# Kernel optimization log

Hardware: AMD Instinct MI355X
Metric: run time of the kernel (lower is better)

The kernel has to match this reference:

```python
import jax, jax.numpy as jnp
import numpy as np

N = 50000      # nodes
E = 800000     # edges (avg degree 16)
IN = 256       # in_feats
H = 128        # hidden_feats
C = 40         # out_feats == num classes (label dim)
LPA_ITERS = 10


def setup_inputs() -> dict:
    key = jax.random.key(0)
    ks = jax.random.split(key, 9)
    features = jax.random.normal(ks[0], (N, IN), dtype=jnp.float32)
    labels = jax.random.normal(ks[1], (N, C), dtype=jnp.float32)
    mask = jax.random.randint(ks[2], (N,), 0, 2) > 0          # bool [N]
    src = jax.random.randint(ks[3], (E,), 0, N, dtype=jnp.int32)
    dst = jax.random.randint(ks[4], (E,), 0, N, dtype=jnp.int32)
    W1 = jax.random.normal(ks[5], (IN, H), dtype=jnp.float32) * (1.0 / np.sqrt(IN))
    b1 = jnp.zeros((H,), dtype=jnp.float32)
    W2 = jax.random.normal(ks[6], (H, C), dtype=jnp.float32) * (1.0 / np.sqrt(H))
    b2 = jnp.zeros((C,), dtype=jnp.float32)
    return {"features": features, "labels": labels, "mask": mask,
            "src": src, "dst": dst, "W1": W1, "b1": b1, "W2": W2, "b2": b2}


def reference(features, labels, mask, src, dst, W1, b1, W2, b2):
    ones_e = jnp.ones((E,), dtype=jnp.float32)
    deg_out = jax.ops.segment_sum(ones_e, src, num_segments=N)  # out-degree
    deg_in = jax.ops.segment_sum(ones_e, dst, num_segments=N)   # in-degree
    norm_src = jnp.maximum(deg_out, 1.0) ** -0.5                 # DGL clamps deg>=1
    norm_dst = jnp.maximum(deg_in, 1.0) ** -0.5

    def gconv(x, W, b):
        # DGL GraphConv, norm='both': D_in^{-1/2} A^T D_out^{-1/2} (x W) + b
        h = (x @ W) * norm_src[:, None]                          # [N, d_out]
        agg = jax.ops.segment_sum(h[src], dst, num_segments=N)   # gather+scatter-add
        return agg * norm_dst[:, None] + b

    x = jax.nn.relu(gconv(features, W1, b1))
    # dropout identity in eval mode
    x = gconv(x, W2, b2)

    # Label propagation: adj[src,dst]=1 so (adj @ y)[i] = sum_{(i->j)} y[j]
    masked_labels = jnp.where(mask[:, None], labels, 0.0)

    def step(y, _):
        y = jax.ops.segment_sum(y[dst], src, num_segments=N)
        y = jnp.where(mask[:, None], labels, y)
        return y, None

    y, _ = jax.lax.scan(step, masked_labels, None, length=LPA_ITERS)
    return x, y
```

## Files before the change

### kernel.cpp

```cpp
#include <hip/hip_runtime.h>

#define Nn 50000
#define Ee 800000
#define INF_ 256
#define HID 128
#define NC 40
#define CAPD 48
#define CAPS 48
#define LPA_ITERS 10
#define NB 98
#define BSH 9
#define EPB 1024
#define NBLK ((Ee + EPB - 1) / EPB)
#define G1_ROWS 64
#define G1BLK ((Nn + G1_ROWS - 1) / G1_ROWS)
#define CAPB_D 10240
#define CAPB_S 6144
#define AGG1_BLKS 2500
#define LPA_BLKS ((Nn + 31) / 32)
#define GEMM2_BLKS ((Nn + 319) / 320)

typedef __attribute__((ext_vector_type(8))) short bfrag;
typedef __attribute__((ext_vector_type(4))) float ffrag;

__device__ inline unsigned f2bf2(float a, float b) {
    unsigned ua = __float_as_uint(a); ua += 0x7FFFu + ((ua >> 16) & 1u);
    unsigned ub = __float_as_uint(b); ub += 0x7FFFu + ((ub >> 16) & 1u);
    return (ua >> 16) | (ub & 0xFFFF0000u);
}
__device__ inline unsigned short f2bf(float a) {
    unsigned ua = __float_as_uint(a); ua += 0x7FFFu + ((ua >> 16) & 1u);
    return (unsigned short)(ua >> 16);
}
__device__ inline float bf_lo(unsigned u) { return __uint_as_float(u << 16); }
__device__ inline float bf_hi(unsigned u) { return __uint_as_float(u & 0xFFFF0000u); }

__device__ inline bool read_mask(const void* mask, int node, int fmt) {
    if (fmt) return ((const unsigned char*)mask)[node] != 0;
    return ((const int*)mask)[node] != 0;
}

__global__ __launch_bounds__(256) void detect_prep(
    const unsigned int* __restrict__ m, int* flag,
    const float* __restrict__ W1, unsigned short* __restrict__ W1t) {
    int bb = blockIdx.x, tid = threadIdx.x;
    if (bb < 49) {
        int i = bb * 256 + tid;
        if (i < 12500) {
            if (m[i] > 1u) atomicOr(flag, 1);
        }
    } else {
        int c = bb - 49;
        W1t[c * INF_ + tid] = f2bf(W1[(size_t)tid * HID + c]);
    }
}

__global__ __launch_bounds__(256) void phase1(
    const int* __restrict__ src, const int* __restrict__ dst,
    const void* __restrict__ mask, const int* __restrict__ flag,
    int* __restrict__ cnt_src, int* __restrict__ cur_d, int* __restrict__ cur_s,
    unsigned* __restrict__ bkt_d, unsigned* __restrict__ bkt_s,
    const float* __restrict__ feat, const unsigned short* __restrict__ W1t,
    unsigned short* __restrict__ h1b) {
    __shared__ uint4 smem[784];
    const int tid = threadIdx.x;
    if (blockIdx.x < NBLK) {
        unsigned* stage_d = (unsigned*)smem;
        unsigned* stage_s = stage_d + EPB;
        int* hd  = (int*)(stage_s + EPB);
        int* od  = hd + NB;
        int* cd  = od + NB + 1;
        int* gd_ = cd + NB;
        int* hs  = gd_ + NB;
// ... 91 lines not shown
        for (int t = 0; t < 8; t++) acc[t] = (ffrag){0.f, 0.f, 0.f, 0.f};

        for (int k0 = 0; k0 < INF_; k0 += 32) {
#pragma unroll
            for (int p = 0; p < 2; p++) {
                int idx = tid + p * 256;
                int r = idx >> 3, c4 = idx & 7;
                int grow = row0 + r;
                float4 v = make_float4(0.f, 0.f, 0.f, 0.f);
                if (grow < Nn)
                    v = *(const float4*)(feat + (size_t)grow * INF_ + k0 + c4 * 4);
                uint2 pk;
                pk.x = f2bf2(v.x, v.y);
                pk.y = f2bf2(v.z, v.w);
                *(uint2*)((char*)lA + r * 64 + c4 * 8) = pk;
            }
#pragma unroll
            for (int p = 0; p < 2; p++) {
                int idx = tid + p * 256;
                int col = idx >> 2, q = idx & 3;
                uint4 v = *(const uint4*)((const char*)W1t + col * 512 + k0 * 2 + q * 16);
                *(uint4*)((char*)lB + col * 64 + q * 16) = v;
            }
            __syncthreads();
            int arow = rw0 + lane15;
            bfrag af = *(const bfrag*)((const char*)lA + arow * 64 + quad * 16);
#pragma unroll
            for (int t = 0; t < 8; t++) {
                int col = t * 16 + lane15;
                bfrag bf = *(const bfrag*)((const char*)lB + col * 64 + quad * 16);
                acc[t] = __builtin_amdgcn_mfma_f32_16x16x32_bf16(af, bf, acc[t], 0, 0, 0);
            }
            __syncthreads();
        }
#pragma unroll
        for (int t = 0; t < 8; t++) {
#pragma unroll
            for (int i = 0; i < 4; i++) {
                int grow = row0 + rw0 + quad * 4 + i;
                if (grow < Nn)
                    h1b[(size_t)grow * HID + t * 16 + lane15] = f2bf(acc[t][i]);
            }
        }
    }
}

__global__ __launch_bounds__(256) void build_csr_both(
    const unsigned* __restrict__ bkt_d, const int* __restrict__ cur_d,
    const unsigned* __restrict__ bkt_s, const int* __restrict__ cur_s,
    const void* __restrict__ mask, const int* __restrict__ flag,
    const int* __restrict__ cnt_src,
    int* __restrict__ adj_dst, int* __restrict__ cnt_dst,
    int* __restrict__ adj_s, int* __restrict__ cnt_u, int* __restrict__ cnt_m,
    float* __restrict__ nrm_s, int* __restrict__ n_un, int* __restrict__ ulist) {
    __shared__ int lu[512], lm[512];
    int bb = blockIdx.x, tid = threadIdx.x;
    lu[tid] = 0; lu[tid + 256] = 0; lm[tid] = 0; lm[tid + 256] = 0;
    __syncthreads();
    if (bb < NB) {
        int b = bb;
        int n = cur_d[b]; if (n > CAPB_D) n = CAPB_D;
        int n0 = b << BSH;
        const unsigned* base = bkt_d + (size_t)b * CAPB_D;
        for (int i = tid; i < n; i += 256) {
            unsigned r = base[i];
            int d = r >> 16, s = r & 0xffff;
            int sl = atomicAdd(&lu[d - n0], 1);
            if (sl < CAPD) adj_dst[d * CAPD + sl] = s;
        }
        __syncthreads();
        int g0 = n0 + tid;
        if (g0 < Nn) cnt_dst[g0] = lu[tid];
        g0 += 256;
        if (g0 < Nn) cnt_dst[g0] = lu[tid + 256];
    } else {
        int b = bb - NB;
        int fmt = *flag;
        int n = cur_s[b]; if (n > CAPB_S) n = CAPB_S;
        int n0 = b << BSH;
        const unsigned* base = bkt_s + (size_t)b * CAPB_S;
        for (int i = tid; i < n; i += 256) {
            unsigned r = base[i];
            int s = r >> 16, d = r & 0xffff;
            if (read_mask(mask, d, fmt)) {
                int sl = atomicAdd(&lm[s - n0], 1);
                if (sl < CAPS) adj_s[s * CAPS + (CAPS - 1 - sl)] = d;
            } else {
                int sl = atomicAdd(&lu[s - n0], 1);
                if (sl < CAPS) adj_s[s * CAPS + sl] = d;
            }
        }
        __syncthreads();
        int g0 = n0 + tid;
        if (g0 < Nn) {
            cnt_u[g0] = lu[tid]; cnt_m[g0] = lm[tid];
            int cs = cnt_src[g0];
            nrm_s[g0] = rsqrtf((float)(cs > 1 ? cs : 1));
            if (!read_mask(mask, g0, fmt)) {
                int p = atomicAdd(n_un, 1);
                ulist[p] = g0;
            }
        }
        g0 += 256;
        if (g0 < Nn) {
            cnt_u[g0] = lu[tid + 256]; cnt_m[g0] = lm[tid + 256];
            int cs = cnt_src[g0];
            nrm_s[g0] = rsqrtf((float)(cs > 1 ? cs : 1));
            if (!read_mask(mask, g0, fmt)) {
                int p = atomicAdd(n_un, 1);
                ulist[p] = g0;
            }
        }
    }
}


__device__ inline void do_agg1(
    int node, int l, const uint4* __restrict__ h1b,
    const int* __restrict__ adj_dst, const int* __restrict__ cnt_dst,
    const float* __restrict__ nrm_s, const float4* __restrict__ b1,
    float4* __restrict__ x1) {
    int dg = cnt_dst[node];
    int cnt = dg < CAPD ? dg : CAPD;
    const int* lst = adj_dst + (size_t)node * CAPD;
    float s0 = 0.f, s1 = 0.f, s2 = 0.f, s3 = 0.f;
    float s4 = 0.f, s5 = 0.f, s6 = 0.f, s7 = 0.f;
    int e = 0;
    for (; e + 8 <= cnt; e += 8) {
        uint4 u[8]; float ns[8];
#pragma unroll
        for (int q = 0; q < 8; q++) {
            int sidx = lst[e + q];
            u[q] = h1b[(size_t)sidx * 16 + l];
            ns[q] = nrm_s[sidx];
        }
#pragma unroll
        for (int q = 0; q < 8; q++) {
            s0 += ns[q] * bf_lo(u[q].x); s1 += ns[q] * bf_hi(u[q].x);
            s2 += ns[q] * bf_lo(u[q].y); s3 += ns[q] * bf_hi(u[q].y);
            s4 += ns[q] * bf_lo(u[q].z); s5 += ns[q] * bf_hi(u[q].z);
            s6 += ns[q] * bf_lo(u[q].w); s7 += ns[q] * bf_hi(u[q].w);
        }
    }
    for (; e < cnt; e++) {
        int sidx = lst[e];
        uint4 u = h1b[(size_t)sidx * 16 + l];
        float nsv = nrm_s[sidx];
        s0 += nsv * bf_lo(u.x); s1 += nsv * bf_hi(u.x);
        s2 += nsv * bf_lo(u.y); s3 += nsv * bf_hi(u.y);
        s4 += nsv * bf_lo(u.z); s5 += nsv * bf_hi(u.z);
        s6 += nsv * bf_lo(u.w); s7 += nsv * bf_hi(u.w);
    }
    float nrm = rsqrtf((float)(dg > 1 ? dg : 1));
    float4 bb0 = b1[l * 2], bb1 = b1[l * 2 + 1];
    float4 v0, v1;
    v0.x = fmaxf(s0 * nrm + bb0.x, 0.f);
    v0.y = fmaxf(s1 * nrm + bb0.y, 0.f);
    v0.z = fmaxf(s2 * nrm + bb0.z, 0.f);
    v0.w = fmaxf(s3 * nrm + bb0.w, 0.f);
    v1.x = fmaxf(s4 * nrm + bb1.x, 0.f);
    v1.y = fmaxf(s5 * nrm + bb1.y, 0.f);
    v1.z = fmaxf(s6 * nrm + bb1.z, 0.f);
    v1.w = fmaxf(s7 * nrm + bb1.w, 0.f);
    x1[(size_t)node * 32 + l * 2] = v0;
    x1[(size_t)node * 32 + l * 2 + 1] = v1;
}

__device__ inline void do_lpa_const(
    int g, int l, const float4* __restrict__ labels,
    const int* __restrict__ ulist, const int* __restrict__ adj_s,
    const int* __restrict__ cnt_m, float4* __restrict__ sconst,
    uint2* __restrict__ y1b) {
    int u = ulist[g];
    int cm = cnt_m[u];
    int cnt = cm < CAPS ? cm : CAPS;
    const int* lst = adj_s + (size_t)u * CAPS + (CAPS - cnt);
    float4 s = make_float4(0.f, 0.f, 0.f, 0.f);
    int e = 0;
    for (; e + 8 <= cnt; e += 8) {
        float4 v[8];
#pragma unroll
        for (int q = 0; q < 8; q++) v[q] = labels[(size_t)lst[e + q] * 10 + l];
#pragma unroll
        for (int q = 0; q < 8; q++) {
            s.x += v[q].x; s.y += v[q].y; s.z += v[q].z; s.w += v[q].w;
        }
    }
    for (; e + 4 <= cnt; e += 4) {
        float4 v[4];
#pragma unroll
        for (int q = 0; q < 4; q++) v[q] = labels[(size_t)lst[e + q] * 10 + l];
#pragma unroll
        for (int q = 0; q < 4; q++) {
            s.x += v[q].x; s.y += v[q].y; s.z += v[q].z; s.w += v[q].w;
        }
    }
    for (; e < cnt; e++) {
        float4 a = labels[(size_t)lst[e] * 10 + l];
        s.x += a.x; s.y += a.y; s.z += a.z; s.w += a.w;
    }
    sconst[(size_t)u * 10 + l] = s;
    uint2 pk; pk.x = f2bf2(s.x, s.y); pk.y = f2bf2(s.z, s.w);
    y1b[(size_t)u * 10 + l] = pk;
}

__device__ inline void do_lpa_mid(
    int g, int l, const uint2* __restrict__ ycur,
    const int* __restrict__ ulist, const int* __restrict__ adj_s,
    const int* __restrict__ cnt_u, const float4* __restrict__ sconst,
    uint2* __restrict__ ynext) {
    int u = ulist[g];
    int cu = cnt_u[u];
    int cnt = cu < CAPS ? cu : CAPS;
    const int* lst = adj_s + (size_t)u * CAPS;
    float4 s = sconst[(size_t)u * 10 + l];
    int e = 0;
    for (; e + 8 <= cnt; e += 8) {
        uint2 v[8];
#pragma unroll
// ... 17 lines not shown
    for (; e < cnt; e++) {
        uint2 v = ycur[(size_t)lst[e] * 10 + l];
        s.x += bf_lo(v.x); s.y += bf_hi(v.x);
        s.z += bf_lo(v.y); s.w += bf_hi(v.y);
    }
    uint2 pk; pk.x = f2bf2(s.x, s.y); pk.y = f2bf2(s.z, s.w);
    ynext[(size_t)u * 10 + l] = pk;
}

__device__ inline void do_agg2(
    int node, int l, const uint2* __restrict__ h2b,
    const int* __restrict__ adj_dst, const int* __restrict__ cnt_dst,
    const float4* __restrict__ b2, float4* __restrict__ out_x) {
    int dg = cnt_dst[node];
    int cnt = dg < CAPD ? dg : CAPD;
    const int* lst = adj_dst + (size_t)node * CAPD;
    float s0 = 0.f, s1 = 0.f, s2 = 0.f, s3 = 0.f;
    int e = 0;
    for (; e + 8 <= cnt; e += 8) {
        uint2 u[8];
#pragma unroll
        for (int q = 0; q < 8; q++) u[q] = h2b[(size_t)lst[e + q] * 10 + l];
#pragma unroll
        for (int q = 0; q < 8; q++) {
            s0 += bf_lo(u[q].x); s1 += bf_hi(u[q].x);
            s2 += bf_lo(u[q].y); s3 += bf_hi(u[q].y);
        }
    }
    for (; e + 4 <= cnt; e += 4) {
        uint2 u[4];
#pragma unroll
        for (int q = 0; q < 4; q++) u[q] = h2b[(size_t)lst[e + q] * 10 + l];
#pragma unroll
        for (int q = 0; q < 4; q++) {
            s0 += bf_lo(u[q].x); s1 += bf_hi(u[q].x);
            s2 += bf_lo(u[q].y); s3 += bf_hi(u[q].y);
        }
    }
    for (; e < cnt; e++) {
        uint2 u = h2b[(size_t)lst[e] * 10 + l];
        s0 += bf_lo(u.x); s1 += bf_hi(u.x);
        s2 += bf_lo(u.y); s3 += bf_hi(u.y);
    }
    float nrm = rsqrtf((float)(dg > 1 ? dg : 1));
    float4 bb = b2[l];
    float4 v;
    v.x = s0 * nrm + bb.x;
    v.y = s1 * nrm + bb.y;
    v.z = s2 * nrm + bb.z;
    v.w = s3 * nrm + bb.w;
    out_x[(size_t)node * 10 + l] = v;
}

__global__ __launch_bounds__(320) void k_agg1_lconst(
    const uint4* __restrict__ h1b, const int* __restrict__ adj_dst,
    const int* __restrict__ cnt_dst, const float* __restrict__ nrm_s,
    const float4* __restrict__ b1, float4* __restrict__ x1,
    const float4* __restrict__ labels, const void* __restrict__ mask,
    const int* __restrict__ flag, const int* __restrict__ n_un,
    const int* __restrict__ ulist, const int* __restrict__ adj_s,
    const int* __restrict__ cnt_m, float4* __restrict__ sconst,
    uint2* __restrict__ y1b, float4* __restrict__ out_y4) {
    int bb = blockIdx.x, tid = threadIdx.x;
    if (bb < AGG1_BLKS) {
        int node = bb * 20 + (tid >> 4);
        do_agg1(node, tid & 15, h1b, adj_dst, cnt_dst, nrm_s, b1, x1);
    } else {
        int lb = bb - AGG1_BLKS;
        int fmt = *flag;
        int i = lb * 320 + tid;
        if (i < Nn * 10) {
            int node = i / 10;
            if (read_mask(mask, node, fmt)) out_y4[i] = labels[i];
        }
        int g = lb * 32 + tid / 10;
        if (g < *n_un)
            do_lpa_const(g, tid % 10, labels, ulist, adj_s, cnt_m, sconst, y1b);
    }
}

__global__ __launch_bounds__(320) void k_gemm2_mid(
    const float4* __restrict__ x1, const float4* __restrict__ W2,
    const int* __restrict__ cnt_src, unsigned* __restrict__ h2b,
    const uint2* __restrict__ ycur, const int* __restrict__ n_un,
    const int* __restrict__ ulist, const int* __restrict__ adj_s,
    const int* __restrict__ cnt_u, const float4* __restrict__ sconst,
    uint2* __restrict__ ynext) {
    __shared__ float lw[HID * NC];
    int bb = blockIdx.x, tid = threadIdx.x;
    if (bb < GEMM2_BLKS) {
        for (int i = tid; i < HID * NC / 4; i += 320)
            ((float4*)lw)[i] = W2[i];
        __syncthreads();
        int r = bb * 320 + tid;
        if (r >= Nn) return;
        const float4* xr = x1 + (size_t)r * 32;
        float4 acc[10];
#pragma unroll
        for (int j = 0; j < 10; j++) acc[j] = make_float4(0.f, 0.f, 0.f, 0.f);
        for (int k4 = 0; k4 < 32; k4++) {
            float4 xv = xr[k4];
#pragma unroll
            for (int s = 0; s < 4; s++) {
                float x = s == 0 ? xv.x : (s == 1 ? xv.y : (s == 2 ? xv.z : xv.w));
                const float4* wrow = (const float4*)(lw + (k4 * 4 + s) * NC);
#pragma unroll
                for (int j = 0; j < 10; j++) {
                    float4 w = wrow[j];
                    acc[j].x += x * w.x; acc[j].y += x * w.y;
                    acc[j].z += x * w.z; acc[j].w += x * w.w;
                }
            }
        }
        int dg = cnt_src[r];
        float nrm = rsqrtf((float)(dg > 1 ? dg : 1));
        uint2* out = (uint2*)(h2b + (size_t)r * 20);
#pragma unroll
        for (int j = 0; j < 10; j++) {
            uint2 pk;
            pk.x = f2bf2(acc[j].x * nrm, acc[j].y * nrm);
            pk.y = f2bf2(acc[j].z * nrm, acc[j].w * nrm);
            out[j] = pk;
        }
    } else {
        int g = (bb - GEMM2_BLKS) * 32 + tid / 10;
        if (g < *n_un)
            do_lpa_mid(g, tid % 10, ycur, ulist, adj_s, cnt_u, sconst, ynext);
    }
}

__global__ __launch_bounds__(320) void k_agg2_mid(
    const uint2* __restrict__ h2b, const int* __restrict__ adj_dst,
    const int* __restrict__ cnt_dst, const float4* __restrict__ b2,
    float4* __restrict__ out_x,
    const uint2* __restrict__ ycur, const int* __restrict__ n_un,
    const int* __restrict__ ulist, const int* __restrict__ adj_s,
    const int* __restrict__ cnt_u, const float4* __restrict__ sconst,
    uint2* __restrict__ ynext) {
    int bb = blockIdx.x, tid = threadIdx.x;
    if (bb < LPA_BLKS) {
        int node = bb * 32 + tid / 10;
        if (node < Nn)
            do_agg2(node, tid % 10, h2b, adj_dst, cnt_dst, b2, out_x);
    } else {
        int g = (bb - LPA_BLKS) * 32 + tid / 10;
        if (g < *n_un)
            do_lpa_mid(g, tid % 10, ycur, ulist, adj_s, cnt_u, sconst, ynext);
    }
}

__global__ __launch_bounds__(320) void lpa_mid(
    const uint2* __restrict__ ycur, const int* __restrict__ n_un,
    const int* __restrict__ ulist, const int* __restrict__ adj_s,
    const int* __restrict__ cnt_u, const float4* __restrict__ sconst,
    uint2* __restrict__ ynext) {
    int g = blockIdx.x * 32 + threadIdx.x / 10;
    if (g < *n_un)
        do_lpa_mid(g, threadIdx.x % 10, ycur, ulist, adj_s, cnt_u, sconst, ynext);
}

__global__ __launch_bounds__(320) void lpa_last(
    const uint2* __restrict__ ycur, const int* __restrict__ n_un,
    const int* __restrict__ ulist, const int* __restrict__ adj_s,
    const int* __restrict__ cnt_u, const float4* __restrict__ sconst,
    float4* __restrict__ out_y) {
    int g = blockIdx.x * 32 + threadIdx.x / 10;
    int l = threadIdx.x % 10;
    if (g >= *n_un) return;
    int u = ulist[g];
    int cu = cnt_u[u];
    int cnt = cu < CAPS ? cu : CAPS;
    const int* lst = adj_s + (size_t)u * CAPS;
    float4 s = sconst[(size_t)u * 10 + l];
    int e = 0;
    for (; e + 8 <= cnt; e += 8) {
        uint2 v[8];
#pragma unroll
        for (int q = 0; q < 8; q++) v[q] = ycur[(size_t)lst[e + q] * 10 + l];
#pragma unroll
        for (int q = 0; q < 8; q++) {
            s.x += bf_lo(v[q].x); s.y += bf_hi(v[q].x);
            s.z += bf_lo(v[q].y); s.w += bf_hi(v[q].y);
        }
    }
    for (; e + 4 <= cnt; e += 4) {
        uint2 v[4];
#pragma unroll
        for (int q = 0; q < 4; q++) v[q] = ycur[(size_t)lst[e + q] * 10 + l];
#pragma unroll
        for (int q = 0; q < 4; q++) {
            s.x += bf_lo(v[q].x); s.y += bf_hi(v[q].x);
            s.z += bf_lo(v[q].y); s.w += bf_hi(v[q].y);
        }
    }
    for (; e < cnt; e++) {
        uint2 v = ycur[(size_t)lst[e] * 10 + l];
        s.x += bf_lo(v.x); s.y += bf_hi(v.x);
        s.z += bf_lo(v.y); s.w += bf_hi(v.y);
    }
    out_y[(size_t)u * 10 + l] = s;
}

extern "C" void kernel_launch(void* const* d_in, const int* in_sizes, int n_in,
                              void* d_out, int out_size, void* d_ws, size_t ws_size,
                              hipStream_t stream) {
    const float* feat   = (const float*)d_in[0];
    const float* labels = (const float*)d_in[1];
    const void*  mask   = d_in[2];
    const int*   src    = (const int*)d_in[3];
    const int*   dst    = (const int*)d_in[4];
    const float* W1     = (const float*)d_in[5];
    const float* b1     = (const float*)d_in[6];
    const float* W2     = (const float*)d_in[7];
    const float* b2     = (const float*)d_in[8];

    float* out_x = (float*)d_out;
    float* out_y = out_x + (size_t)Nn * NC;

    char* ws = (char*)d_ws;
    size_t off = 0;
    auto alloc = [&](size_t bytes) -> void* {
        void* p = ws + off;
        off += (bytes + 255) & ~(size_t)255;
        return p;
    };
    int* flag    = (int*)alloc(256);
    int* n_un    = flag + 1;
    int* cnt_src = (int*)alloc((size_t)Nn * 4);
    int* cur_d   = (int*)alloc(512);
    int* cur_s   = (int*)alloc(512);
    size_t zero_bytes = off;
    int* cnt_dst = (int*)alloc((size_t)Nn * 4);
    int* cnt_u   = (int*)alloc((size_t)Nn * 4);
    int* cnt_m   = (int*)alloc((size_t)Nn * 4);
    int* ulist   = (int*)alloc((size_t)Nn * 4);
    float* nrm_s = (float*)alloc((size_t)Nn * 4);
    unsigned short* W1t = (unsigned short*)alloc((size_t)HID * INF_ * 2);
    unsigned* bkt_d = (unsigned*)alloc((size_t)NB * CAPB_D * 4);
    unsigned* bkt_s = (unsigned*)alloc((size_t)NB * CAPB_S * 4);
    unsigned short* h1b = (unsigned short*)alloc((size_t)Nn * HID * 2);
    float* x1 = (float*)alloc((size_t)Nn * HID * 4);
    int* adj_s   = (int*)alloc((size_t)Nn * CAPS * 4);
    int* adj_dst = (int*)alloc((size_t)Nn * CAPD * 4);
    unsigned* h2b = (unsigned*)alloc((size_t)Nn * NC * 2);
    float* sconst = (float*)alloc((size_t)Nn * NC * 4);
    uint2* y1b = (uint2*)alloc((size_t)Nn * NC * 2);
    uint2* y2b = (uint2*)alloc((size_t)Nn * NC * 2);

    hipMemsetAsync(d_ws, 0, zero_bytes, stream);

    detect_prep<<<49 + HID, 256, 0, stream>>>((const unsigned int*)mask, flag,
                                              W1, W1t);
    phase1<<<NBLK + G1BLK, 256, 0, stream>>>(
        src, dst, mask, flag, cnt_src, cur_d, cur_s, bkt_d, bkt_s,
        feat, W1t, h1b);
    build_csr_both<<<NB * 2, 256, 0, stream>>>(
        bkt_d, cur_d, bkt_s, cur_s, mask, flag, cnt_src,
        adj_dst, cnt_dst, adj_s, cnt_u, cnt_m, nrm_s, n_un, ulist);

    k_agg1_lconst<<<AGG1_BLKS + LPA_BLKS, 320, 0, stream>>>(
        (const uint4*)h1b, adj_dst, cnt_dst, nrm_s, (const float4*)b1,
        (float4*)x1, (const float4*)labels, mask, flag, n_un, ulist, adj_s,
        cnt_m, (float4*)sconst, y1b, (float4*)out_y);
    k_gemm2_mid<<<GEMM2_BLKS + LPA_BLKS, 320, 0, stream>>>(
        (const float4*)x1, (const float4*)W2, cnt_src, h2b,
        y1b, n_un, ulist, adj_s, cnt_u, (const float4*)sconst, y2b);
    k_agg2_mid<<<LPA_BLKS + LPA_BLKS, 320, 0, stream>>>(
        (const uint2*)h2b, adj_dst, cnt_dst, (const float4*)b2, (float4*)out_x,
        y2b, n_un, ulist, adj_s, cnt_u, (const float4*)sconst, y1b);

    const uint2* cur = y1b;
    for (int i = 0; i < 6; i++) {
        uint2* nxt = (i & 1) ? y1b : y2b;
        lpa_mid<<<LPA_BLKS, 320, 0, stream>>>(
            cur, n_un, ulist, adj_s, cnt_u, (const float4*)sconst, nxt);
        cur = nxt;
    }
    lpa_last<<<LPA_BLKS, 320, 0, stream>>>(
        cur, n_un, ulist, adj_s, cnt_u, (const float4*)sconst, (float4*)out_y);
}
```

Baseline: 375.1 us.

## Fuse remaining LPA iterations into one cooperative kernel with grid sync

Replaces the six lpa_mid launches and the final lpa_last launch with one cooperative kernel. It runs a fixed grid of 768 blocks that loops over the unlabeled nodes and uses grid.sync() between iterations, ping-ponging the y buffers. This removes per-launch overhead and the drain and refill gaps between seven small kernels. In exchange it uses fewer resident blocks with grid-stride loops, and grid-wide barriers could reduce latency hiding for the gather-bound work.

```diff
diff --git a/kernel.cpp b/kernel.cpp
--- a/kernel.cpp
+++ b/kernel.cpp
@@ -1,4 +1,7 @@
 #include <hip/hip_runtime.h>
+#include <hip/hip_cooperative_groups.h>
+
+namespace cg = cooperative_groups;
 
 #define Nn 50000
 #define Ee 800000
@@ -19,6 +22,7 @@
 #define AGG1_BLKS 2500
 #define LPA_BLKS ((Nn + 31) / 32)
 #define GEMM2_BLKS ((Nn + 319) / 320)
+#define COOP_BLKS 768
 
 typedef __attribute__((ext_vector_type(8))) short bfrag;
 typedef __attribute__((ext_vector_type(4))) float ffrag;
@@ -549,56 +553,61 @@
     }
 }
 
-__global__ __launch_bounds__(320) void lpa_mid(
-    const uint2* __restrict__ ycur, const int* __restrict__ n_un,
-    const int* __restrict__ ulist, const int* __restrict__ adj_s,
-    const int* __restrict__ cnt_u, const float4* __restrict__ sconst,
-    uint2* __restrict__ ynext) {
-    int g = blockIdx.x * 32 + threadIdx.x / 10;
-    if (g < *n_un)
-        do_lpa_mid(g, threadIdx.x % 10, ycur, ulist, adj_s, cnt_u, sconst, ynext);
-}
-
-__global__ __launch_bounds__(320) void lpa_last(
-    const uint2* __restrict__ ycur, const int* __restrict__ n_un,
-    const int* __restrict__ ulist, const int* __restrict__ adj_s,
-    const int* __restrict__ cnt_u, const float4* __restrict__ sconst,
+__global__ __launch_bounds__(320) void lpa_coop(
+    const int* __restrict__ n_un, const int* __restrict__ ulist,
+    const int* __restrict__ adj_s, const int* __restrict__ cnt_u,
+    const float4* __restrict__ sconst,
+    uint2* __restrict__ ya, uint2* __restrict__ yb,
     float4* __restrict__ out_y) {
-    int g = blockIdx.x * 32 + threadIdx.x / 10;
-    int l = threadIdx.x % 10;
-    if (g >= *n_un) return;
-    int u = ulist[g];
-    int cu = cnt_u[u];
-    int cnt = cu < CAPS ? cu : CAPS;
-    const int* lst = adj_s + (size_t)u * CAPS;
-    float4 s = sconst[(size_t)u * 10 + l];
-    int e = 0;
-    for (; e + 8 <= cnt; e += 8) {
-        uint2 v[8];
-#pragma unroll
-        for (int q = 0; q < 8; q++) v[q] = ycur[(size_t)lst[e + q] * 10 + l];
-#pragma unroll
-        for (int q = 0; q < 8; q++) {
-            s.x += bf_lo(v[q].x); s.y += bf_hi(v[q].x);
-            s.z += bf_lo(v[q].y); s.w += bf_hi(v[q].y);
-        }
-    }
-    for (; e + 4 <= cnt; e += 4) {
-        uint2 v[4];
-#pragma unroll
-        for (int q = 0; q < 4; q++) v[q] = ycur[(size_t)lst[e + q] * 10 + l];
-#pragma unroll
-        for (int q = 0; q < 4; q++) {
-            s.x += bf_lo(v[q].x); s.y += bf_hi(v[q].x);
-            s.z += bf_lo(v[q].y); s.w += bf_hi(v[q].y);
-        }
-    }
-    for (; e < cnt; e++) {
-        uint2 v = ycur[(size_t)lst[e] * 10 + l];
-        s.x += bf_lo(v.x); s.y += bf_hi(v.x);
-        s.z += bf_lo(v.y); s.w += bf_hi(v.y);
-    }
-    out_y[(size_t)u * 10 + l] = s;
+    cg::grid_group grid = cg::this_grid();
+    const int nu = *n_un;
+    const int l = threadIdx.x % 10;
+    const int g0 = blockIdx.x * 32 + threadIdx.x / 10;
+    const int gstep = gridDim.x * 32;
+
+    const uint2* cur = ya;
+    uint2* nxt = yb;
+#pragma unroll 1
+    for (int it = 0; it < 6; it++) {
+        for (int g = g0; g < nu; g += gstep)
+            do_lpa_mid(g, l, cur, ulist, adj_s, cnt_u, sconst, nxt);
+        grid.sync();
+        const uint2* t = cur; cur = nxt; nxt = (uint2*)t;
+    }
+    for (int g = g0; g < nu; g += gstep) {
+        int u = ulist[g];
+        int cu = cnt_u[u];
+        int cnt = cu < CAPS ? cu : CAPS;
+        const int* lst = adj_s + (size_t)u * CAPS;
+        float4 s = sconst[(size_t)u * 10 + l];
+        int e = 0;
+        for (; e + 8 <= cnt; e += 8) {
+            uint2 v[8];
+#pragma unroll
+            for (int q = 0; q < 8; q++) v[q] = cur[(size_t)lst[e + q] * 10 + l];
+#pragma unroll
+            for (int q = 0; q < 8; q++) {
+                s.x += bf_lo(v[q].x); s.y += bf_hi(v[q].x);
+                s.z += bf_lo(v[q].y); s.w += bf_hi(v[q].y);
+            }
+        }
+        for (; e + 4 <= cnt; e += 4) {
+            uint2 v[4];
+#pragma unroll
+            for (int q = 0; q < 4; q++) v[q] = cur[(size_t)lst[e + q] * 10 + l];
+#pragma unroll
+            for (int q = 0; q < 4; q++) {
+                s.x += bf_lo(v[q].x); s.y += bf_hi(v[q].x);
+                s.z += bf_lo(v[q].y); s.w += bf_hi(v[q].y);
+            }
+        }
+        for (; e < cnt; e++) {
+            uint2 v = cur[(size_t)lst[e] * 10 + l];
+            s.x += bf_lo(v.x); s.y += bf_hi(v.x);
+            s.z += bf_lo(v.y); s.w += bf_hi(v.y);
+        }
+        out_y[(size_t)u * 10 + l] = s;
+    }
 }
 
 extern "C" void kernel_launch(void* const* d_in, const int* in_sizes, int n_in,
@@ -669,13 +678,17 @@
         (const uint2*)h2b, adj_dst, cnt_dst, (const float4*)b2, (float4*)out_x,
         y2b, n_un, ulist, adj_s, cnt_u, (const float4*)sconst, y1b);
 
-    const uint2* cur = y1b;
-    for (int i = 0; i < 6; i++) {
-        uint2* nxt = (i & 1) ? y1b : y2b;
-        lpa_mid<<<LPA_BLKS, 320, 0, stream>>>(
-            cur, n_un, ulist, adj_s, cnt_u, (const float4*)sconst, nxt);
-        cur = nxt;
-    }
-    lpa_last<<<LPA_BLKS, 320, 0, stream>>>(
-        cur, n_un, ulist, adj_s, cnt_u, (const float4*)sconst, (float4*)out_y);
-}
+    const int* n_un_c = n_un;
+    const int* ulist_c = ulist;
+    const int* adj_s_c = adj_s;
+    const int* cnt_u_c = cnt_u;
+    const float4* sconst_c = (const float4*)sconst;
+    uint2* ya = y1b;
+    uint2* yb = y2b;
+    float4* outy4 = (float4*)out_y;
+    void* cargs[] = {(void*)&n_un_c, (void*)&ulist_c, (void*)&adj_s_c,
+                     (void*)&cnt_u_c, (void*)&sconst_c, (void*)&ya,
+                     (void*)&yb, (void*)&outy4};
+    hipLaunchCooperativeKernel((void*)lpa_coop, dim3(COOP_BLKS), dim3(320),
+                               cargs, 0, stream);
+}
```

Measured after the change: 914.5 us. 2.44x slower.

## Fuse layer-1 aggregation with layer-2 GEMM and prescale h1 by source norm

Applied to the files above, without the earlier changes.

The layer-1 aggregation kernel now also computes the 128x40 W2 projection in shared memory per block of 20 nodes and writes bf16 h2 directly. This removes the fp32 x1 intermediate and the separate gemm2 kernel. The source-degree normalization is folded into h1 by extra blocks in the CSR build kernel, so the gather no longer loads nrm_s per edge. The LPA iteration that ran inside gemm2 is moved into the loop as an extra lpa_mid launch. The costs are an extra round of bf16 rounding on h1 and per-block W2 staging into shared memory, which raises LDS use and may lower occupancy.

```diff
diff --git a/kernel.cpp b/kernel.cpp
--- a/kernel.cpp
+++ b/kernel.cpp
@@ -18,7 +18,7 @@
 #define CAPB_S 6144
 #define AGG1_BLKS 2500
 #define LPA_BLKS ((Nn + 31) / 32)
-#define GEMM2_BLKS ((Nn + 319) / 320)
+#define SCB 196
 
 typedef __attribute__((ext_vector_type(8))) short bfrag;
 typedef __attribute__((ext_vector_type(4))) float ffrag;
@@ -216,7 +216,8 @@
     const int* __restrict__ cnt_src,
     int* __restrict__ adj_dst, int* __restrict__ cnt_dst,
     int* __restrict__ adj_s, int* __restrict__ cnt_u, int* __restrict__ cnt_m,
-    float* __restrict__ nrm_s, int* __restrict__ n_un, int* __restrict__ ulist) {
+    int* __restrict__ n_un, int* __restrict__ ulist,
+    unsigned short* __restrict__ h1b) {
     __shared__ int lu[512], lm[512];
     int bb = blockIdx.x, tid = threadIdx.x;
     lu[tid] = 0; lu[tid + 256] = 0; lm[tid] = 0; lm[tid + 256] = 0;
@@ -237,7 +238,7 @@
         if (g0 < Nn) cnt_dst[g0] = lu[tid];
         g0 += 256;
         if (g0 < Nn) cnt_dst[g0] = lu[tid + 256];
-    } else {
+    } else if (bb < 2 * NB) {
         int b = bb - NB;
         int fmt = *flag;
         int n = cur_s[b]; if (n > CAPB_S) n = CAPB_S;
@@ -258,8 +259,6 @@
         int g0 = n0 + tid;
         if (g0 < Nn) {
             cnt_u[g0] = lu[tid]; cnt_m[g0] = lm[tid];
-            int cs = cnt_src[g0];
-            nrm_s[g0] = rsqrtf((float)(cs > 1 ? cs : 1));
             if (!read_mask(mask, g0, fmt)) {
                 int p = atomicAdd(n_un, 1);
                 ulist[p] = g0;
@@ -268,67 +267,35 @@
         g0 += 256;
         if (g0 < Nn) {
             cnt_u[g0] = lu[tid + 256]; cnt_m[g0] = lm[tid + 256];
-            int cs = cnt_src[g0];
-            nrm_s[g0] = rsqrtf((float)(cs > 1 ? cs : 1));
             if (!read_mask(mask, g0, fmt)) {
                 int p = atomicAdd(n_un, 1);
                 ulist[p] = g0;
             }
         }
-    }
-}
-
-
-__device__ inline void do_agg1(
-    int node, int l, const uint4* __restrict__ h1b,
-    const int* __restrict__ adj_dst, const int* __restrict__ cnt_dst,
-    const float* __restrict__ nrm_s, const float4* __restrict__ b1,
-    float4* __restrict__ x1) {
-    int dg = cnt_dst[node];
-    int cnt = dg < CAPD ? dg : CAPD;
-    const int* lst = adj_dst + (size_t)node * CAPD;
-    float s0 = 0.f, s1 = 0.f, s2 = 0.f, s3 = 0.f;
-    float s4 = 0.f, s5 = 0.f, s6 = 0.f, s7 = 0.f;
-    int e = 0;
-    for (; e + 8 <= cnt; e += 8) {
-        uint4 u[8]; float ns[8];
-#pragma unroll
-        for (int q = 0; q < 8; q++) {
-            int sidx = lst[e + q];
-            u[q] = h1b[(size_t)sidx * 16 + l];
-            ns[q] = nrm_s[sidx];
-        }
-#pragma unroll
-        for (int q = 0; q < 8; q++) {
-            s0 += ns[q] * bf_lo(u[q].x); s1 += ns[q] * bf_hi(u[q].x);
-            s2 += ns[q] * bf_lo(u[q].y); s3 += ns[q] * bf_hi(u[q].y);
-            s4 += ns[q] * bf_lo(u[q].z); s5 += ns[q] * bf_hi(u[q].z);
-            s6 += ns[q] * bf_lo(u[q].w); s7 += ns[q] * bf_hi(u[q].w);
-        }
-    }
-    for (; e < cnt; e++) {
-        int sidx = lst[e];
-        uint4 u = h1b[(size_t)sidx * 16 + l];
-        float nsv = nrm_s[sidx];
-        s0 += nsv * bf_lo(u.x); s1 += nsv * bf_hi(u.x);
-        s2 += nsv * bf_lo(u.y); s3 += nsv * bf_hi(u.y);
-        s4 += nsv * bf_lo(u.z); s5 += nsv * bf_hi(u.z);
-        s6 += nsv * bf_lo(u.w); s7 += nsv * bf_hi(u.w);
-    }
-    float nrm = rsqrtf((float)(dg > 1 ? dg : 1));
-    float4 bb0 = b1[l * 2], bb1 = b1[l * 2 + 1];
-    float4 v0, v1;
-    v0.x = fmaxf(s0 * nrm + bb0.x, 0.f);
-    v0.y = fmaxf(s1 * nrm + bb0.y, 0.f);
-    v0.z = fmaxf(s2 * nrm + bb0.z, 0.f);
-    v0.w = fmaxf(s3 * nrm + bb0.w, 0.f);
-    v1.x = fmaxf(s4 * nrm + bb1.x, 0.f);
-    v1.y = fmaxf(s5 * nrm + bb1.y, 0.f);
-    v1.z = fmaxf(s6 * nrm + bb1.z, 0.f);
-    v1.w = fmaxf(s7 * nrm + bb1.w, 0.f);
-    x1[(size_t)node * 32 + l * 2] = v0;
-    x1[(size_t)node * 32 + l * 2 + 1] = v1;
-}
+    } else {
+        int b = bb - 2 * NB;
+        int rbase = b * 256;
+        int c8 = tid & 7;
+#pragma unroll 1
+        for (int it = 0; it < 8; it++) {
+            int r = rbase + it * 32 + (tid >> 3);
+            if (r >= Nn) continue;
+            int cs = cnt_src[r];
+            float nr = rsqrtf((float)(cs > 1 ? cs : 1));
+            uint4* row = (uint4*)(h1b + (size_t)r * HID);
+#pragma unroll
+            for (int h = 0; h < 2; h++) {
+                uint4 u = row[c8 * 2 + h];
+                u.x = f2bf2(bf_lo(u.x) * nr, bf_hi(u.x) * nr);
+                u.y = f2bf2(bf_lo(u.y) * nr, bf_hi(u.y) * nr);
+                u.z = f2bf2(bf_lo(u.z) * nr, bf_hi(u.z) * nr);
+                u.w = f2bf2(bf_lo(u.w) * nr, bf_hi(u.w) * nr);
+                row[c8 * 2 + h] = u;
+            }
+        }
+    }
+}
+
 
 __device__ inline void do_lpa_const(
     int g, int l, const float4* __restrict__ labels,
@@ -452,19 +419,96 @@
     out_x[(size_t)node * 10 + l] = v;
 }
 
-__global__ __launch_bounds__(320) void k_agg1_lconst(
+__global__ __launch_bounds__(320) void k_aggemm_lconst(
     const uint4* __restrict__ h1b, const int* __restrict__ adj_dst,
-    const int* __restrict__ cnt_dst, const float* __restrict__ nrm_s,
-    const float4* __restrict__ b1, float4* __restrict__ x1,
+    const int* __restrict__ cnt_dst, const int* __restrict__ cnt_src,
+    const float4* __restrict__ b1, const float* __restrict__ W2,
+    unsigned* __restrict__ h2b,
     const float4* __restrict__ labels, const void* __restrict__ mask,
     const int* __restrict__ flag, const int* __restrict__ n_un,
     const int* __restrict__ ulist, const int* __restrict__ adj_s,
     const int* __restrict__ cnt_m, float4* __restrict__ sconst,
     uint2* __restrict__ y1b, float4* __restrict__ out_y4) {
+    __shared__ float lsm[NC * 132 + 20 * 132];
     int bb = blockIdx.x, tid = threadIdx.x;
     if (bb < AGG1_BLKS) {
-        int node = bb * 20 + (tid >> 4);
-        do_agg1(node, tid & 15, h1b, adj_dst, cnt_dst, nrm_s, b1, x1);
+        float* lwt = lsm;
+        float* xs  = lsm + NC * 132;
+        for (int i = tid; i < HID * NC; i += 320) {
+            int k = i / NC, c = i % NC;
+            lwt[c * 132 + k] = W2[i];
+        }
+        __syncthreads();
+
+        const int slot = tid >> 4;
+        const int node = bb * 20 + slot;
+        const int l = tid & 15;
+        int dg = cnt_dst[node];
+        int cnt = dg < CAPD ? dg : CAPD;
+        const int* lst = adj_dst + (size_t)node * CAPD;
+        float s0 = 0.f, s1 = 0.f, s2 = 0.f, s3 = 0.f;
+        float s4 = 0.f, s5 = 0.f, s6 = 0.f, s7 = 0.f;
+        int e = 0;
+        for (; e + 8 <= cnt; e += 8) {
+            uint4 u[8];
+#pragma unroll
+            for (int q = 0; q < 8; q++) u[q] = h1b[(size_t)lst[e + q] * 16 + l];
+#pragma unroll
+            for (int q = 0; q < 8; q++) {
+                s0 += bf_lo(u[q].x); s1 += bf_hi(u[q].x);
+                s2 += bf_lo(u[q].y); s3 += bf_hi(u[q].y);
+                s4 += bf_lo(u[q].z); s5 += bf_hi(u[q].z);
+                s6 += bf_lo(u[q].w); s7 += bf_hi(u[q].w);
+            }
+        }
+        for (; e < cnt; e++) {
+            uint4 u = h1b[(size_t)lst[e] * 16 + l];
+            s0 += bf_lo(u.x); s1 += bf_hi(u.x);
+            s2 += bf_lo(u.y); s3 += bf_hi(u.y);
+            s4 += bf_lo(u.z); s5 += bf_hi(u.z);
+            s6 += bf_lo(u.w); s7 += bf_hi(u.w);
+        }
+        float nrm = rsqrtf((float)(dg > 1 ? dg : 1));
+        float4 bb0 = b1[l * 2], bb1 = b1[l * 2 + 1];
+        float4 v0, v1;
+        v0.x = fmaxf(s0 * nrm + bb0.x, 0.f);
+        v0.y = fmaxf(s1 * nrm + bb0.y, 0.f);
+        v0.z = fmaxf(s2 * nrm + bb0.z, 0.f);
+        v0.w = fmaxf(s3 * nrm + bb0.w, 0.f);
+        v1.x = fmaxf(s4 * nrm + bb1.x, 0.f);
+        v1.y = fmaxf(s5 * nrm + bb1.y, 0.f);
+        v1.z = fmaxf(s6 * nrm + bb1.z, 0.f);
+        v1.w = fmaxf(s7 * nrm + bb1.w, 0.f);
+        float* xrow = xs + slot * 132;
+        *(float4*)(xrow + l * 8) = v0;
+        *(float4*)(xrow + l * 8 + 4) = v1;
+        __syncthreads();
+
+        int c0 = l, c1 = l + 16;
+        const float* w0 = lwt + c0 * 132;
+        const float* w1 = lwt + c1 * 132;
+        const float* w2p = lwt + ((l < 8) ? (l + 32) : c0) * 132;
+        float a0 = 0.f, a1 = 0.f, a2 = 0.f;
+#pragma unroll 8
+        for (int k4 = 0; k4 < 32; k4++) {
+            float4 xv = *(const float4*)(xrow + k4 * 4);
+            float4 wa = *(const float4*)(w0 + k4 * 4);
+            float4 wb = *(const float4*)(w1 + k4 * 4);
+            float4 wc = *(const float4*)(w2p + k4 * 4);
+            a0 += xv.x * wa.x + xv.y * wa.y + xv.z * wa.z + xv.w * wa.w;
+            a1 += xv.x * wb.x + xv.y * wb.y + xv.z * wb.z + xv.w * wb.w;
+            a2 += xv.x * wc.x + xv.y * wc.y + xv.z * wc.z + xv.w * wc.w;
+        }
+        int dgs = cnt_src[node];
+        float nrm2 = rsqrtf((float)(dgs > 1 ? dgs : 1));
+        xrow[c0] = a0 * nrm2;
+        xrow[c1] = a1 * nrm2;
+        if (l < 8) xrow[l + 32] = a2 * nrm2;
+        if (l < 10) {
+            float4 p = *(const float4*)(xrow + l * 4);
+            uint2 pk; pk.x = f2bf2(p.x, p.y); pk.y = f2bf2(p.z, p.w);
+            ((uint2*)(h2b + (size_t)node * 20))[l] = pk;
+        }
     } else {
         int lb = bb - AGG1_BLKS;
         int fmt = *flag;
@@ -476,56 +520,6 @@
         int g = lb * 32 + tid / 10;
         if (g < *n_un)
             do_lpa_const(g, tid % 10, labels, ulist, adj_s, cnt_m, sconst, y1b);
-    }
-}
-
-__global__ __launch_bounds__(320) void k_gemm2_mid(
-    const float4* __restrict__ x1, const float4* __restrict__ W2,
-    const int* __restrict__ cnt_src, unsigned* __restrict__ h2b,
-    const uint2* __restrict__ ycur, const int* __restrict__ n_un,
-    const int* __restrict__ ulist, const int* __restrict__ adj_s,
-    const int* __restrict__ cnt_u, const float4* __restrict__ sconst,
-    uint2* __restrict__ ynext) {
-    __shared__ float lw[HID * NC];
-    int bb = blockIdx.x, tid = threadIdx.x;
-    if (bb < GEMM2_BLKS) {
-        for (int i = tid; i < HID * NC / 4; i += 320)
-            ((float4*)lw)[i] = W2[i];
-        __syncthreads();
-        int r = bb * 320 + tid;
-        if (r >= Nn) return;
-        const float4* xr = x1 + (size_t)r * 32;
-        float4 acc[10];
-#pragma unroll
-        for (int j = 0; j < 10; j++) acc[j] = make_float4(0.f, 0.f, 0.f, 0.f);
-        for (int k4 = 0; k4 < 32; k4++) {
-            float4 xv = xr[k4];
-#pragma unroll
-            for (int s = 0; s < 4; s++) {
-                float x = s == 0 ? xv.x : (s == 1 ? xv.y : (s == 2 ? xv.z : xv.w));
-                const float4* wrow = (const float4*)(lw + (k4 * 4 + s) * NC);
-#pragma unroll
-                for (int j = 0; j < 10; j++) {
-                    float4 w = wrow[j];
-                    acc[j].x += x * w.x; acc[j].y += x * w.y;
-                    acc[j].z += x * w.z; acc[j].w += x * w.w;
-                }
-            }
-        }
-        int dg = cnt_src[r];
-        float nrm = rsqrtf((float)(dg > 1 ? dg : 1));
-        uint2* out = (uint2*)(h2b + (size_t)r * 20);
-#pragma unroll
-        for (int j = 0; j < 10; j++) {
-            uint2 pk;
-            pk.x = f2bf2(acc[j].x * nrm, acc[j].y * nrm);
-            pk.y = f2bf2(acc[j].z * nrm, acc[j].w * nrm);
-            out[j] = pk;
-        }
-    } else {
-        int g = (bb - GEMM2_BLKS) * 32 + tid / 10;
-        if (g < *n_un)
-            do_lpa_mid(g, tid % 10, ycur, ulist, adj_s, cnt_u, sconst, ynext);
     }
 }
 
@@ -634,12 +628,10 @@
     int* cnt_u   = (int*)alloc((size_t)Nn * 4);
     int* cnt_m   = (int*)alloc((size_t)Nn * 4);
     int* ulist   = (int*)alloc((size_t)Nn * 4);
-    float* nrm_s = (float*)alloc((size_t)Nn * 4);
     unsigned short* W1t = (unsigned short*)alloc((size_t)HID * INF_ * 2);
     unsigned* bkt_d = (unsigned*)alloc((size_t)NB * CAPB_D * 4);
     unsigned* bkt_s = (unsigned*)alloc((size_t)NB * CAPB_S * 4);
     unsigned short* h1b = (unsigned short*)alloc((size_t)Nn * HID * 2);
-    float* x1 = (float*)alloc((size_t)Nn * HID * 4);
     int* adj_s   = (int*)alloc((size_t)Nn * CAPS * 4);
     int* adj_dst = (int*)alloc((size_t)Nn * CAPD * 4);
     unsigned* h2b = (unsigned*)alloc((size_t)Nn * NC * 2);
@@ -654,24 +646,21 @@
     phase1<<<NBLK + G1BLK, 256, 0, stream>>>(
         src, dst, mask, flag, cnt_src, cur_d, cur_s, bkt_d, bkt_s,
         feat, W1t, h1b);
-    build_csr_both<<<NB * 2, 256, 0, stream>>>(
+    build_csr_both<<<NB * 2 + SCB, 256, 0, stream>>>(
         bkt_d, cur_d, bkt_s, cur_s, mask, flag, cnt_src,
-        adj_dst, cnt_dst, adj_s, cnt_u, cnt_m, nrm_s, n_un, ulist);
-
-    k_agg1_lconst<<<AGG1_BLKS + LPA_BLKS, 320, 0, stream>>>(
-        (const uint4*)h1b, adj_dst, cnt_dst, nrm_s, (const float4*)b1,
-        (float4*)x1, (const float4*)labels, mask, flag, n_un, ulist, adj_s,
+        adj_dst, cnt_dst, adj_s, cnt_u, cnt_m, n_un, ulist, h1b);
+
+    k_aggemm_lconst<<<AGG1_BLKS + LPA_BLKS, 320, 0, stream>>>(
+        (const uint4*)h1b, adj_dst, cnt_dst, cnt_src, (const float4*)b1,
+        W2, h2b, (const float4*)labels, mask, flag, n_un, ulist, adj_s,
         cnt_m, (float4*)sconst, y1b, (float4*)out_y);
-    k_gemm2_mid<<<GEMM2_BLKS + LPA_BLKS, 320, 0, stream>>>(
-        (const float4*)x1, (const float4*)W2, cnt_src, h2b,
-        y1b, n_un, ulist, adj_s, cnt_u, (const float4*)sconst, y2b);
     k_agg2_mid<<<LPA_BLKS + LPA_BLKS, 320, 0, stream>>>(
         (const uint2*)h2b, adj_dst, cnt_dst, (const float4*)b2, (float4*)out_x,
-        y2b, n_un, ulist, adj_s, cnt_u, (const float4*)sconst, y1b);
-
-    const uint2* cur = y1b;
-    for (int i = 0; i < 6; i++) {
-        uint2* nxt = (i & 1) ? y1b : y2b;
+        y1b, n_un, ulist, adj_s, cnt_u, (const float4*)sconst, y2b);
+
+    const uint2* cur = y2b;
+    for (int i = 0; i < 7; i++) {
+        uint2* nxt = (i & 1) ? y2b : y1b;
         lpa_mid<<<LPA_BLKS, 320, 0, stream>>>(
             cur, n_un, ulist, adj_s, cnt_u, (const float4*)sconst, nxt);
         cur = nxt;
```

Result: faster. 367.7 us (-2.0%).

## Prescale h1 by source norm in place and store layer-1 activations as bf16

Applied to the files above, without the earlier changes.

Extra blocks in the CSR build kernel scale each bf16 h1 row in place by the source-degree norm. This removes the per-edge nrm_s gather from the layer-1 aggregation and drops the nrm_s array. The layer-1 output x1 is now written and read as bf16 instead of fp32, which halves its write and read traffic into the second GEMM. The cost is an extra read-modify-write pass over h1 and additional bf16 rounding, both on the prescaled h1 and on x1.

```diff
diff --git a/kernel.cpp b/kernel.cpp
--- a/kernel.cpp
+++ b/kernel.cpp
@@ -19,6 +19,7 @@
 #define AGG1_BLKS 2500
 #define LPA_BLKS ((Nn + 31) / 32)
 #define GEMM2_BLKS ((Nn + 319) / 320)
+#define SCB 196
 
 typedef __attribute__((ext_vector_type(8))) short bfrag;
 typedef __attribute__((ext_vector_type(4))) float ffrag;
@@ -216,7 +217,8 @@
     const int* __restrict__ cnt_src,
     int* __restrict__ adj_dst, int* __restrict__ cnt_dst,
     int* __restrict__ adj_s, int* __restrict__ cnt_u, int* __restrict__ cnt_m,
-    float* __restrict__ nrm_s, int* __restrict__ n_un, int* __restrict__ ulist) {
+    int* __restrict__ n_un, int* __restrict__ ulist,
+    unsigned short* __restrict__ h1b) {
     __shared__ int lu[512], lm[512];
     int bb = blockIdx.x, tid = threadIdx.x;
     lu[tid] = 0; lu[tid + 256] = 0; lm[tid] = 0; lm[tid + 256] = 0;
@@ -237,7 +239,7 @@
         if (g0 < Nn) cnt_dst[g0] = lu[tid];
         g0 += 256;
         if (g0 < Nn) cnt_dst[g0] = lu[tid + 256];
-    } else {
+    } else if (bb < 2 * NB) {
         int b = bb - NB;
         int fmt = *flag;
         int n = cur_s[b]; if (n > CAPB_S) n = CAPB_S;
@@ -258,8 +260,6 @@
         int g0 = n0 + tid;
         if (g0 < Nn) {
             cnt_u[g0] = lu[tid]; cnt_m[g0] = lm[tid];
-            int cs = cnt_src[g0];
-            nrm_s[g0] = rsqrtf((float)(cs > 1 ? cs : 1));
             if (!read_mask(mask, g0, fmt)) {
                 int p = atomicAdd(n_un, 1);
                 ulist[p] = g0;
@@ -268,67 +268,35 @@
         g0 += 256;
         if (g0 < Nn) {
             cnt_u[g0] = lu[tid + 256]; cnt_m[g0] = lm[tid + 256];
-            int cs = cnt_src[g0];
-            nrm_s[g0] = rsqrtf((float)(cs > 1 ? cs : 1));
             if (!read_mask(mask, g0, fmt)) {
                 int p = atomicAdd(n_un, 1);
                 ulist[p] = g0;
             }
         }
-    }
-}
-
-
-__device__ inline void do_agg1(
-    int node, int l, const uint4* __restrict__ h1b,
-    const int* __restrict__ adj_dst, const int* __restrict__ cnt_dst,
-    const float* __restrict__ nrm_s, const float4* __restrict__ b1,
-    float4* __restrict__ x1) {
-    int dg = cnt_dst[node];
-    int cnt = dg < CAPD ? dg : CAPD;
-    const int* lst = adj_dst + (size_t)node * CAPD;
-    float s0 = 0.f, s1 = 0.f, s2 = 0.f, s3 = 0.f;
-    float s4 = 0.f, s5 = 0.f, s6 = 0.f, s7 = 0.f;
-    int e = 0;
-    for (; e + 8 <= cnt; e += 8) {
-        uint4 u[8]; float ns[8];
-#pragma unroll
-        for (int q = 0; q < 8; q++) {
-            int sidx = lst[e + q];
-            u[q] = h1b[(size_t)sidx * 16 + l];
-            ns[q] = nrm_s[sidx];
-        }
-#pragma unroll
-        for (int q = 0; q < 8; q++) {
-            s0 += ns[q] * bf_lo(u[q].x); s1 += ns[q] * bf_hi(u[q].x);
-            s2 += ns[q] * bf_lo(u[q].y); s3 += ns[q] * bf_hi(u[q].y);
-            s4 += ns[q] * bf_lo(u[q].z); s5 += ns[q] * bf_hi(u[q].z);
-            s6 += ns[q] * bf_lo(u[q].w); s7 += ns[q] * bf_hi(u[q].w);
-        }
-    }
-    for (; e < cnt; e++) {
-        int sidx = lst[e];
-        uint4 u = h1b[(size_t)sidx * 16 + l];
-        float nsv = nrm_s[sidx];
-        s0 += nsv * bf_lo(u.x); s1 += nsv * bf_hi(u.x);
-        s2 += nsv * bf_lo(u.y); s3 += nsv * bf_hi(u.y);
-        s4 += nsv * bf_lo(u.z); s5 += nsv * bf_hi(u.z);
-        s6 += nsv * bf_lo(u.w); s7 += nsv * bf_hi(u.w);
-    }
-    float nrm = rsqrtf((float)(dg > 1 ? dg : 1));
-    float4 bb0 = b1[l * 2], bb1 = b1[l * 2 + 1];
-    float4 v0, v1;
-    v0.x = fmaxf(s0 * nrm + bb0.x, 0.f);
-    v0.y = fmaxf(s1 * nrm + bb0.y, 0.f);
-    v0.z = fmaxf(s2 * nrm + bb0.z, 0.f);
-    v0.w = fmaxf(s3 * nrm + bb0.w, 0.f);
-    v1.x = fmaxf(s4 * nrm + bb1.x, 0.f);
-    v1.y = fmaxf(s5 * nrm + bb1.y, 0.f);
-    v1.z = fmaxf(s6 * nrm + bb1.z, 0.f);
-    v1.w = fmaxf(s7 * nrm + bb1.w, 0.f);
-    x1[(size_t)node * 32 + l * 2] = v0;
-    x1[(size_t)node * 32 + l * 2 + 1] = v1;
-}
+    } else {
+        int b = bb - 2 * NB;
+        int rbase = b * 256;
+        int c8 = tid & 7;
+#pragma unroll 1
+        for (int it = 0; it < 8; it++) {
+            int r = rbase + it * 32 + (tid >> 3);
+            if (r >= Nn) continue;
+            int cs = cnt_src[r];
+            float nr = rsqrtf((float)(cs > 1 ? cs : 1));
+            uint4* row = (uint4*)(h1b + (size_t)r * HID);
+#pragma unroll
+            for (int h = 0; h < 2; h++) {
+                uint4 u = row[c8 * 2 + h];
+                u.x = f2bf2(bf_lo(u.x) * nr, bf_hi(u.x) * nr);
+                u.y = f2bf2(bf_lo(u.y) * nr, bf_hi(u.y) * nr);
+                u.z = f2bf2(bf_lo(u.z) * nr, bf_hi(u.z) * nr);
+                u.w = f2bf2(bf_lo(u.w) * nr, bf_hi(u.w) * nr);
+                row[c8 * 2 + h] = u;
+            }
+        }
+    }
+}
+
 
 __device__ inline void do_lpa_const(
     int g, int l, const float4* __restrict__ labels,
@@ -454,8 +422,8 @@
 
 __global__ __launch_bounds__(320) void k_agg1_lconst(
     const uint4* __restrict__ h1b, const int* __restrict__ adj_dst,
-    const int* __restrict__ cnt_dst, const float* __restrict__ nrm_s,
-    const float4* __restrict__ b1, float4* __restrict__ x1,
+    const int* __restrict__ cnt_dst, const float4* __restrict__ b1,
+    uint4* __restrict__ x1b,
     const float4* __restrict__ labels, const void* __restrict__ mask,
     const int* __restrict__ flag, const int* __restrict__ n_un,
     const int* __restrict__ ulist, const int* __restrict__ adj_s,
@@ -463,8 +431,49 @@
     uint2* __restrict__ y1b, float4* __restrict__ out_y4) {
     int bb = blockIdx.x, tid = threadIdx.x;
     if (bb < AGG1_BLKS) {
-        int node = bb * 20 + (tid >> 4);
-        do_agg1(node, tid & 15, h1b, adj_dst, cnt_dst, nrm_s, b1, x1);
+        const int node = bb * 20 + (tid >> 4);
+        const int l = tid & 15;
+        int dg = cnt_dst[node];
+        int cnt = dg < CAPD ? dg : CAPD;
+        const int* lst = adj_dst + (size_t)node * CAPD;
+        float s0 = 0.f, s1 = 0.f, s2 = 0.f, s3 = 0.f;
+        float s4 = 0.f, s5 = 0.f, s6 = 0.f, s7 = 0.f;
+        int e = 0;
+        for (; e + 8 <= cnt; e += 8) {
+            uint4 u[8];
+#pragma unroll
+            for (int q = 0; q < 8; q++) u[q] = h1b[(size_t)lst[e + q] * 16 + l];
+#pragma unroll
+            for (int q = 0; q < 8; q++) {
+                s0 += bf_lo(u[q].x); s1 += bf_hi(u[q].x);
+                s2 += bf_lo(u[q].y); s3 += bf_hi(u[q].y);
+                s4 += bf_lo(u[q].z); s5 += bf_hi(u[q].z);
+                s6 += bf_lo(u[q].w); s7 += bf_hi(u[q].w);
+            }
+        }
+        for (; e < cnt; e++) {
+            uint4 u = h1b[(size_t)lst[e] * 16 + l];
+            s0 += bf_lo(u.x); s1 += bf_hi(u.x);
+            s2 += bf_lo(u.y); s3 += bf_hi(u.y);
+            s4 += bf_lo(u.z); s5 += bf_hi(u.z);
+            s6 += bf_lo(u.w); s7 += bf_hi(u.w);
+        }
+        float nrm = rsqrtf((float)(dg > 1 ? dg : 1));
+        float4 bb0 = b1[l * 2], bb1 = b1[l * 2 + 1];
+        float v0x = fmaxf(s0 * nrm + bb0.x, 0.f);
+        float v0y = fmaxf(s1 * nrm + bb0.y, 0.f);
+        float v0z = fmaxf(s2 * nrm + bb0.z, 0.f);
+        float v0w = fmaxf(s3 * nrm + bb0.w, 0.f);
+        float v1x = fmaxf(s4 * nrm + bb1.x, 0.f);
+        float v1y = fmaxf(s5 * nrm + bb1.y, 0.f);
+        float v1z = fmaxf(s6 * nrm + bb1.z, 0.f);
+        float v1w = fmaxf(s7 * nrm + bb1.w, 0.f);
+        uint4 pk4;
+        pk4.x = f2bf2(v0x, v0y);
+        pk4.y = f2bf2(v0z, v0w);
+        pk4.z = f2bf2(v1x, v1y);
+        pk4.w = f2bf2(v1z, v1w);
+        x1b[(size_t)node * 16 + l] = pk4;
     } else {
         int lb = bb - AGG1_BLKS;
         int fmt = *flag;
@@ -480,7 +489,7 @@
 }
 
 __global__ __launch_bounds__(320) void k_gemm2_mid(
-    const float4* __restrict__ x1, const float4* __restrict__ W2,
+    const uint4* __restrict__ x1b, const float4* __restrict__ W2,
     const int* __restrict__ cnt_src, unsigned* __restrict__ h2b,
     const uint2* __restrict__ ycur, const int* __restrict__ n_un,
     const int* __restrict__ ulist, const int* __restrict__ adj_s,
@@ -494,16 +503,21 @@
         __syncthreads();
         int r = bb * 320 + tid;
         if (r >= Nn) return;
-        const float4* xr = x1 + (size_t)r * 32;
+        const uint4* xr = x1b + (size_t)r * 16;
         float4 acc[10];
 #pragma unroll
         for (int j = 0; j < 10; j++) acc[j] = make_float4(0.f, 0.f, 0.f, 0.f);
-        for (int k4 = 0; k4 < 32; k4++) {
-            float4 xv = xr[k4];
-#pragma unroll
-            for (int s = 0; s < 4; s++) {
-                float x = s == 0 ? xv.x : (s == 1 ? xv.y : (s == 2 ? xv.z : xv.w));
-                const float4* wrow = (const float4*)(lw + (k4 * 4 + s) * NC);
+        for (int kk = 0; kk < 16; kk++) {
+            uint4 u = xr[kk];
+            float xv[8];
+            xv[0] = bf_lo(u.x); xv[1] = bf_hi(u.x);
+            xv[2] = bf_lo(u.y); xv[3] = bf_hi(u.y);
+            xv[4] = bf_lo(u.z); xv[5] = bf_hi(u.z);
+            xv[6] = bf_lo(u.w); xv[7] = bf_hi(u.w);
+#pragma unroll
+            for (int s = 0; s < 8; s++) {
+                float x = xv[s];
+                const float4* wrow = (const float4*)(lw + (kk * 8 + s) * NC);
 #pragma unroll
                 for (int j = 0; j < 10; j++) {
                     float4 w = wrow[j];
@@ -634,12 +648,11 @@
     int* cnt_u   = (int*)alloc((size_t)Nn * 4);
     int* cnt_m   = (int*)alloc((size_t)Nn * 4);
     int* ulist   = (int*)alloc((size_t)Nn * 4);
-    float* nrm_s = (float*)alloc((size_t)Nn * 4);
     unsigned short* W1t = (unsigned short*)alloc((size_t)HID * INF_ * 2);
     unsigned* bkt_d = (unsigned*)alloc((size_t)NB * CAPB_D * 4);
     unsigned* bkt_s = (unsigned*)alloc((size_t)NB * CAPB_S * 4);
     unsigned short* h1b = (unsigned short*)alloc((size_t)Nn * HID * 2);
-    float* x1 = (float*)alloc((size_t)Nn * HID * 4);
+    uint4* x1b = (uint4*)alloc((size_t)Nn * HID * 2);
     int* adj_s   = (int*)alloc((size_t)Nn * CAPS * 4);
     int* adj_dst = (int*)alloc((size_t)Nn * CAPD * 4);
     unsigned* h2b = (unsigned*)alloc((size_t)Nn * NC * 2);
@@ -654,16 +667,16 @@
     phase1<<<NBLK + G1BLK, 256, 0, stream>>>(
         src, dst, mask, flag, cnt_src, cur_d, cur_s, bkt_d, bkt_s,
         feat, W1t, h1b);
-    build_csr_both<<<NB * 2, 256, 0, stream>>>(
+    build_csr_both<<<NB * 2 + SCB, 256, 0, stream>>>(
         bkt_d, cur_d, bkt_s, cur_s, mask, flag, cnt_src,
-        adj_dst, cnt_dst, adj_s, cnt_u, cnt_m, nrm_s, n_un, ulist);
+        adj_dst, cnt_dst, adj_s, cnt_u, cnt_m, n_un, ulist, h1b);
 
     k_agg1_lconst<<<AGG1_BLKS + LPA_BLKS, 320, 0, stream>>>(
-        (const uint4*)h1b, adj_dst, cnt_dst, nrm_s, (const float4*)b1,
-        (float4*)x1, (const float4*)labels, mask, flag, n_un, ulist, adj_s,
+        (const uint4*)h1b, adj_dst, cnt_dst, (const float4*)b1, x1b,
+        (const float4*)labels, mask, flag, n_un, ulist, adj_s,
         cnt_m, (float4*)sconst, y1b, (float4*)out_y);
     k_gemm2_mid<<<GEMM2_BLKS + LPA_BLKS, 320, 0, stream>>>(
-        (const float4*)x1, (const float4*)W2, cnt_src, h2b,
+        (const uint4*)x1b, (const float4*)W2, cnt_src, h2b,
         y1b, n_un, ulist, adj_s, cnt_u, (const float4*)sconst, y2b);
     k_agg2_mid<<<LPA_BLKS + LPA_BLKS, 320, 0, stream>>>(
         (const uint2*)h2b, adj_dst, cnt_dst, (const float4*)b2, (float4*)out_x,
```

Result: faster. 362.7 us, median of 3 (-3.3%).
